# Kernel optimization log

Measured on AMD Instinct MI355X. Metric: run time of the kernel, lower is better.

Reference implementation:

```python
import jax, jax.numpy as jnp
import numpy as np

D_IN = 1024
D_OUT = 1024
NUM_HEADS = 16
HEAD_DIM = D_OUT // NUM_HEADS


def setup_inputs() -> dict:
    key = jax.random.key(0)
    ks = jax.random.split(key, 6)
    s = 0.02
    return {
        "x": jax.random.normal(ks[0], (4, 2048, D_IN), dtype=jnp.float32),
        "Wq": jax.random.normal(ks[1], (D_IN, D_OUT), dtype=jnp.float32) * s,
        "Wk": jax.random.normal(ks[2], (D_IN, D_OUT), dtype=jnp.float32) * s,
        "Wv": jax.random.normal(ks[3], (D_IN, D_OUT), dtype=jnp.float32) * s,
        "Wo": jax.random.normal(ks[4], (D_OUT, D_OUT), dtype=jnp.float32) * s,
        "bo": jax.random.normal(ks[5], (D_OUT,), dtype=jnp.float32) * s,
    }


def reference(x, Wq, Wk, Wv, Wo, bo):
    B, S, _ = x.shape
    # QKV projections (no bias), split into heads: [B, H, S, Dh]
    def split_heads(t):
        return t.reshape(B, S, NUM_HEADS, HEAD_DIM).transpose(0, 2, 1, 3)

    q = split_heads(x @ Wq)
    k = split_heads(x @ Wk)
    v = split_heads(x @ Wv)

    # causal scores [B, H, S, S]; note: original masks BEFORE scaling,
    # but -inf is scale-invariant so softmax(scores/sqrt(d)) with mask is identical.
    scores = jnp.einsum("bhqd,bhkd->bhqk", q, k) / jnp.sqrt(jnp.asarray(HEAD_DIM, x.dtype))
    causal = jnp.tril(jnp.ones((S, S), dtype=bool))
    scores = jnp.where(causal, scores, -jnp.inf)
    attn = jax.nn.softmax(scores, axis=-1)
    # dropout p=0.0 -> identity
    ctx = jnp.einsum("bhqk,bhkd->bhqd", attn, v)  # [B, H, S, Dh]
    ctx = ctx.transpose(0, 2, 1, 3).reshape(B, S, D_OUT)
    return ctx @ Wo + bo
```

## Files before the change

kernel.cpp:

```cpp
#include <hip/hip_runtime.h>
#include <hip/hip_bf16.h>
#include <math.h>


typedef __attribute__((ext_vector_type(8))) short short8;
typedef __attribute__((ext_vector_type(4))) float f32x4;

#define MFMA_BF16(a, b, c) __builtin_amdgcn_mfma_f32_16x16x32_bf16((a), (b), (c), 0, 0, 0)

__device__ __forceinline__ void gld_lds16(const void* g, void* l) {
  __builtin_amdgcn_global_load_lds((const __attribute__((address_space(1))) void*)g,
                                   (__attribute__((address_space(3))) void*)l, 16, 0, 0);
}

__global__ void cast_f32_bf16(const float* __restrict__ in, __hip_bfloat16* __restrict__ out) {
  int i = blockIdx.x * blockDim.x + threadIdx.x;
  float4 v = ((const float4*)in)[i];
  __align__(8) __hip_bfloat16 tmp[4] = {__float2bfloat16(v.x), __float2bfloat16(v.y),
                                        __float2bfloat16(v.z), __float2bfloat16(v.w)};
  ((ushort4*)out)[i] = *(const ushort4*)tmp;
}

__global__ void transpose_cast_w4(const float* __restrict__ W0, const float* __restrict__ W1,
                                  const float* __restrict__ W2, const float* __restrict__ W3,
                                  __hip_bfloat16* __restrict__ T0, __hip_bfloat16* __restrict__ T1,
                                  __hip_bfloat16* __restrict__ T2, __hip_bfloat16* __restrict__ T3) {
  const int z = blockIdx.z;
  const float* W = (z == 0) ? W0 : (z == 1) ? W1 : (z == 2) ? W2 : W3;
  __hip_bfloat16* Wt = (z == 0) ? T0 : (z == 1) ? T1 : (z == 2) ? T2 : T3;
  __shared__ float tile[32][33];
  int tx = threadIdx.x, ty = threadIdx.y;
  int n0 = blockIdx.x * 32, k0 = blockIdx.y * 32;
#pragma unroll
  for (int i = 0; i < 4; ++i)
    tile[ty + i * 8][tx] = W[(size_t)(k0 + ty + i * 8) * 1024 + n0 + tx];
  __syncthreads();
#pragma unroll
  for (int i = 0; i < 4; ++i)
    Wt[(size_t)(n0 + ty + i * 8) * 1024 + k0 + tx] = __float2bfloat16(tile[tx][ty + i * 8]);
}

__global__ __launch_bounds__(256, 2) void gemm_qkv(
    const __hip_bfloat16* __restrict__ A, const __hip_bfloat16* __restrict__ Bt,
    __hip_bfloat16* __restrict__ q, __hip_bfloat16* __restrict__ k,
    __hip_bfloat16* __restrict__ vT) {
  __shared__ __align__(16) __hip_bfloat16 As[128 * 32];
  __shared__ __align__(16) __hip_bfloat16 Bs[128 * 32];
  const int tid = threadIdx.x;
  const int lane = tid & 63, wid = tid >> 6;
  const int quad = lane >> 4, l16 = lane & 15;
  const int part = blockIdx.x >> 3;
  const int n0 = (blockIdx.x & 7) * 128;
  const int gn0 = part * 1024 + n0;
  const int m0 = blockIdx.y * 128;
  const int wm = (wid & 1) * 64, wn = (wid >> 1) * 64;

  f32x4 acc[4][4] = {};

  for (int k0 = 0; k0 < 1024; k0 += 32) {
    __syncthreads();
#pragma unroll
    for (int i = 0; i < 2; ++i) {
      int sbase = __builtin_amdgcn_readfirstlane(wid * 64 + i * 256);
      int s = sbase + lane;
      int row = s >> 2, ch = s & 3;
      gld_lds16(A + (size_t)(m0 + row) * 1024 + k0 + ch * 8, &As[sbase * 8]);
      gld_lds16(Bt + (size_t)(gn0 + row) * 1024 + k0 + ch * 8, &Bs[sbase * 8]);
    }
    __syncthreads();

    short8 af[4], bfr[4];
#pragma unroll
    for (int t = 0; t < 4; ++t) {
      af[t] = *(const short8*)&As[(wm + t * 16 + l16) * 32 + quad * 8];
      bfr[t] = *(const short8*)&Bs[(wn + t * 16 + l16) * 32 + quad * 8];
    }
#pragma unroll
    for (int mt = 0; mt < 4; ++mt)
#pragma unroll
      for (int nt = 0; nt < 4; ++nt)
        acc[mt][nt] = MFMA_BF16(af[mt], bfr[nt], acc[mt][nt]);
  }

  const float CSCL = 0.18033688011112042f;
  if (part < 2) {
    __hip_bfloat16* C = (part == 0) ? q : k;
    const float scl = (part == 0) ? CSCL : 1.0f;
#pragma unroll
    for (int mt = 0; mt < 4; ++mt)
#pragma unroll
      for (int nt = 0; nt < 4; ++nt) {
        int row = m0 + wm + mt * 16 + quad * 4;
        int col = n0 + wn + nt * 16 + l16;
#pragma unroll
        for (int r = 0; r < 4; ++r)
          C[(size_t)(row + r) * 1024 + col] = __float2bfloat16(acc[mt][nt][r] * scl);
      }
  } else {
#pragma unroll
    for (int mt = 0; mt < 4; ++mt)
#pragma unroll
      for (int nt = 0; nt < 4; ++nt) {
        int row = m0 + wm + mt * 16 + quad * 4;
        int nn = n0 + wn + nt * 16 + l16;
        __align__(8) __hip_bfloat16 p4[4];
#pragma unroll
        for (int r = 0; r < 4; ++r) p4[r] = __float2bfloat16(acc[mt][nt][r]);
        *(ushort4*)(vT + (size_t)nn * 8192 + row) = *(const ushort4*)p4;
      }
  }
}

__global__ __launch_bounds__(256, 2) void gemm_bt_f32out(
    const __hip_bfloat16* __restrict__ A, const __hip_bfloat16* __restrict__ Bt,
    float* __restrict__ C, const float* __restrict__ bias, int M, int N, int K) {
  __shared__ __align__(16) __hip_bfloat16 As[128 * 32];
  __shared__ __align__(16) __hip_bfloat16 Bs[128 * 32];
  const int tid = threadIdx.x;
  const int lane = tid & 63, wid = tid >> 6;
  const int quad = lane >> 4, l16 = lane & 15;
  const int m0 = blockIdx.y * 128, n0 = blockIdx.x * 128;
  const int wm = (wid & 1) * 64, wn = (wid >> 1) * 64;

  f32x4 acc[4][4] = {};

  for (int k0 = 0; k0 < K; k0 += 32) {
    __syncthreads();
#pragma unroll
    for (int i = 0; i < 2; ++i) {
      int sbase = __builtin_amdgcn_readfirstlane(wid * 64 + i * 256);
      int s = sbase + lane;
      int row = s >> 2, ch = s & 3;
      gld_lds16(A + (size_t)(m0 + row) * K + k0 + ch * 8, &As[sbase * 8]);
      gld_lds16(Bt + (size_t)(n0 + row) * K + k0 + ch * 8, &Bs[sbase * 8]);
    }
    __syncthreads();

    short8 af[4], bfr[4];
#pragma unroll
    for (int t = 0; t < 4; ++t) {
      af[t] = *(const short8*)&As[(wm + t * 16 + l16) * 32 + quad * 8];
      bfr[t] = *(const short8*)&Bs[(wn + t * 16 + l16) * 32 + quad * 8];
    }
#pragma unroll
    for (int mt = 0; mt < 4; ++mt)
#pragma unroll
      for (int nt = 0; nt < 4; ++nt)
        acc[mt][nt] = MFMA_BF16(af[mt], bfr[nt], acc[mt][nt]);
  }

#pragma unroll
  for (int mt = 0; mt < 4; ++mt)
#pragma unroll
    for (int nt = 0; nt < 4; ++nt) {
      int row = m0 + wm + mt * 16 + quad * 4;
      int col = n0 + wn + nt * 16 + l16;
      float b = bias[col];
#pragma unroll
      for (int r = 0; r < 4; ++r)
        C[(size_t)(row + r) * N + col] = acc[mt][nt][r] + b;
    }
}

__global__ __launch_bounds__(256, 2) void attn_kernel(
    const __hip_bfloat16* __restrict__ Q, const __hip_bfloat16* __restrict__ Km,
    const __hip_bfloat16* __restrict__ vT, __hip_bfloat16* __restrict__ ctx) {
  const int bid = blockIdx.x;
  const int p = bid & 7, h = (bid >> 3) & 15, b = bid >> 7;
  const size_t rbase = (size_t)b * 2048;
  const int tid = threadIdx.x, lane = tid & 63, wid = tid >> 6;
  const int quad = lane >> 4, l16 = lane & 15;

  __shared__ __align__(16) __hip_bfloat16 Ks[64 * 72];
  __shared__ __align__(16) __hip_bfloat16 Vs[64 * 72];
  __shared__ __align__(16) __hip_bfloat16 Ps[4][32 * 76];

  const float NEG_BIG = -1e30f;

#pragma unroll 1
  for (int sub = 0; sub < 2; ++sub) {
    const int qt = sub ? (15 - p) : p;
    const int q0 = qt * 128;

    short8 qf[2][2];
#pragma unroll
    for (int mt = 0; mt < 2; ++mt)
#pragma unroll
      for (int kc = 0; kc < 2; ++kc)
        qf[mt][kc] = *(const short8*)(Q + (rbase + q0 + wid * 32 + mt * 16 + l16) * 1024 +
                                      h * 64 + kc * 32 + quad * 8);

    f32x4 o[2][4] = {};
    f32x4 lp[2] = {};
    const int wave_max_row = q0 + wid * 32 + 31;
    const int ktiles = q0 / 64 + 2;

#pragma unroll 1
    for (int kt = 0; kt < ktiles; ++kt) {
      const int kbase = kt * 64;
      __syncthreads();
      {
#pragma unroll
        for (int i = 0; i < 2; ++i) {
          int s = tid + i * 256;
          int krow = s >> 3, ch = s & 7;
          *(short8*)&Ks[krow * 72 + ch * 8] =
              *(const short8*)(Km + (rbase + kbase + krow) * 1024 + h * 64 + ch * 8);
        }
      }
      {
#pragma unroll
        for (int i = 0; i < 2; ++i) {
          int s = tid + i * 256;
          int d = s >> 3, ch = s & 7;
          *(short8*)&Vs[d * 72 + ch * 8] =
              *(const short8*)(vT + (size_t)(h * 64 + d) * 8192 + rbase + kbase + ch * 8);
        }
      }
      __syncthreads();

      if (kbase <= wave_max_row) {
        short8 kf[4][2];
#pragma unroll
        for (int nt = 0; nt < 4; ++nt)
#pragma unroll
          for (int kc = 0; kc < 2; ++kc)
            kf[nt][kc] = *(const short8*)&Ks[(nt * 16 + l16) * 72 + kc * 32 + quad * 8];
        f32x4 s[2][4];
#pragma unroll
        for (int mt = 0; mt < 2; ++mt)
#pragma unroll
          for (int nt = 0; nt < 4; ++nt) {
            f32x4 sv = {0.f, 0.f, 0.f, 0.f};
            sv = MFMA_BF16(qf[mt][0], kf[nt][0], sv);
            sv = MFMA_BF16(qf[mt][1], kf[nt][1], sv);
            s[mt][nt] = sv;
          }
        if (kbase + 63 > q0 + wid * 32) {
#pragma unroll
          for (int mt = 0; mt < 2; ++mt)
#pragma unroll
            for (int nt = 0; nt < 4; ++nt)
#pragma unroll
              for (int r = 0; r < 4; ++r) {
                int row = q0 + wid * 32 + mt * 16 + quad * 4 + r;
                int col = kbase + nt * 16 + l16;
                if (col > row) s[mt][nt][r] = NEG_BIG;
              }
        }
#pragma unroll
        for (int mt = 0; mt < 2; ++mt) {
#pragma unroll
          for (int nt = 0; nt < 4; ++nt)
#pragma unroll
            for (int r = 0; r < 4; ++r) {
              float pv = __builtin_amdgcn_exp2f(s[mt][nt][r]);
              s[mt][nt][r] = pv;
              lp[mt][r] += pv;
            }
#pragma unroll
          for (int nt = 0; nt < 4; ++nt)
#pragma unroll
            for (int r = 0; r < 4; ++r)
              Ps[wid][(mt * 16 + quad * 4 + r) * 76 + nt * 16 + l16] =
                  __float2bfloat16(s[mt][nt][r]);
        }
        short8 pa[2][2], vf[4][2];
#pragma unroll
        for (int mt = 0; mt < 2; ++mt)
#pragma unroll
          for (int ch = 0; ch < 2; ++ch)
            pa[mt][ch] = *(const short8*)&Ps[wid][(mt * 16 + l16) * 76 + ch * 32 + quad * 8];
#pragma unroll
        for (int dt = 0; dt < 4; ++dt)
#pragma unroll
          for (int ch = 0; ch < 2; ++ch)
            vf[dt][ch] = *(const short8*)&Vs[(dt * 16 + l16) * 72 + ch * 32 + quad * 8];
#pragma unroll
        for (int mt = 0; mt < 2; ++mt)
#pragma unroll
          for (int dt = 0; dt < 4; ++dt) {
            o[mt][dt] = MFMA_BF16(pa[mt][0], vf[dt][0], o[mt][dt]);
            o[mt][dt] = MFMA_BF16(pa[mt][1], vf[dt][1], o[mt][dt]);
          }
      }
    }

#pragma unroll
    for (int mt = 0; mt < 2; ++mt) {
#pragma unroll
      for (int msk = 1; msk <= 8; msk <<= 1)
#pragma unroll
        for (int r = 0; r < 4; ++r)
          lp[mt][r] += __shfl_xor(lp[mt][r], msk, 64);
      float inv[4];
#pragma unroll
      for (int r = 0; r < 4; ++r) inv[r] = 1.f / lp[mt][r];
#pragma unroll
      for (int dt = 0; dt < 4; ++dt)
#pragma unroll
        for (int r = 0; r < 4; ++r)
          ctx[(rbase + q0 + wid * 32 + mt * 16 + quad * 4 + r) * 1024 + h * 64 + dt * 16 + l16] =
              __float2bfloat16(o[mt][dt][r] * inv[r]);
    }
  }
}

extern "C" void kernel_launch(void* const* d_in, const int* in_sizes, int n_in,
                              void* d_out, int out_size, void* d_ws, size_t ws_size,
                              hipStream_t stream) {
  const float* x  = (const float*)d_in[0];
  const float* Wq = (const float*)d_in[1];
  const float* Wk = (const float*)d_in[2];
  const float* Wv = (const float*)d_in[3];
  const float* Wo = (const float*)d_in[4];
  const float* bo = (const float*)d_in[5];
  float* out = (float*)d_out;

  char* ws = (char*)d_ws;
  const size_t MB = 1024ull * 1024ull;
  __hip_bfloat16* q   = (__hip_bfloat16*)(ws);
  __hip_bfloat16* k   = (__hip_bfloat16*)(ws + 16 * MB);
  __hip_bfloat16* vT  = (__hip_bfloat16*)(ws + 32 * MB);
  __hip_bfloat16* woT = (__hip_bfloat16*)(ws + 48 * MB);
  __hip_bfloat16* ctx = q;

  char* outc = (char*)d_out;
  __hip_bfloat16* xb    = (__hip_bfloat16*)(outc);
  __hip_bfloat16* wcatT = (__hip_bfloat16*)(outc + 16 * MB);

  cast_f32_bf16<<<8192, 256, 0, stream>>>(x, xb);
  transpose_cast_w4<<<dim3(32, 32, 4), dim3(32, 8), 0, stream>>>(
      Wq, Wk, Wv, Wo, wcatT, wcatT + 1024 * 1024, wcatT + 2048 * 1024, woT);

  gemm_qkv<<<dim3(24, 64), 256, 0, stream>>>(xb, wcatT, q, k, vT);

  attn_kernel<<<512, 256, 0, stream>>>(q, k, vT, ctx);

  gemm_bt_f32out<<<dim3(8, 64), 256, 0, stream>>>(ctx, woT, out, bo, 8192, 1024, 1024);
}
```

Before: 260.9 us.

## Double GEMM K-tile to 64 with XOR-swizzled LDS and fuse prep kernels

Both bf16 GEMMs now stage 64-wide K slices per iteration instead of 32, halving the number of barrier pairs per tile. An XOR swizzle on the 16-byte chunk index is applied both when loading into LDS and when reading fragments, to avoid bank conflicts caused by the wider row stride. Separately, the x cast and the weight transpose-cast are merged into one launch to save a kernel launch. LDS use per block doubles, which may affect occupancy under the two-blocks-per-CU bound.

```diff
diff --git a/kernel.cpp b/kernel.cpp
--- a/kernel.cpp
+++ b/kernel.cpp
@@ -13,39 +13,42 @@
                                    (__attribute__((address_space(3))) void*)l, 16, 0, 0);
 }
 
-__global__ void cast_f32_bf16(const float* __restrict__ in, __hip_bfloat16* __restrict__ out) {
-  int i = blockIdx.x * blockDim.x + threadIdx.x;
-  float4 v = ((const float4*)in)[i];
-  __align__(8) __hip_bfloat16 tmp[4] = {__float2bfloat16(v.x), __float2bfloat16(v.y),
-                                        __float2bfloat16(v.z), __float2bfloat16(v.w)};
-  ((ushort4*)out)[i] = *(const ushort4*)tmp;
-}
-
-__global__ void transpose_cast_w4(const float* __restrict__ W0, const float* __restrict__ W1,
-                                  const float* __restrict__ W2, const float* __restrict__ W3,
-                                  __hip_bfloat16* __restrict__ T0, __hip_bfloat16* __restrict__ T1,
-                                  __hip_bfloat16* __restrict__ T2, __hip_bfloat16* __restrict__ T3) {
-  const int z = blockIdx.z;
-  const float* W = (z == 0) ? W0 : (z == 1) ? W1 : (z == 2) ? W2 : W3;
-  __hip_bfloat16* Wt = (z == 0) ? T0 : (z == 1) ? T1 : (z == 2) ? T2 : T3;
-  __shared__ float tile[32][33];
-  int tx = threadIdx.x, ty = threadIdx.y;
-  int n0 = blockIdx.x * 32, k0 = blockIdx.y * 32;
-#pragma unroll
-  for (int i = 0; i < 4; ++i)
-    tile[ty + i * 8][tx] = W[(size_t)(k0 + ty + i * 8) * 1024 + n0 + tx];
-  __syncthreads();
-#pragma unroll
-  for (int i = 0; i < 4; ++i)
-    Wt[(size_t)(n0 + ty + i * 8) * 1024 + k0 + tx] = __float2bfloat16(tile[tx][ty + i * 8]);
+__global__ void prep_kernel(const float* __restrict__ x, __hip_bfloat16* __restrict__ xb,
+                            const float* __restrict__ W0, const float* __restrict__ W1,
+                            const float* __restrict__ W2, const float* __restrict__ W3,
+                            __hip_bfloat16* __restrict__ T0, __hip_bfloat16* __restrict__ T1,
+                            __hip_bfloat16* __restrict__ T2, __hip_bfloat16* __restrict__ T3) {
+  const int bid = blockIdx.x, tid = threadIdx.x;
+  if (bid < 8192) {
+    int i = bid * 256 + tid;
+    float4 v = ((const float4*)x)[i];
+    __align__(8) __hip_bfloat16 tmp[4] = {__float2bfloat16(v.x), __float2bfloat16(v.y),
+                                          __float2bfloat16(v.z), __float2bfloat16(v.w)};
+    ((ushort4*)xb)[i] = *(const ushort4*)tmp;
+  } else {
+    int zz = bid - 8192;
+    int z = zz >> 10, rem = zz & 1023;
+    const float* W = (z == 0) ? W0 : (z == 1) ? W1 : (z == 2) ? W2 : W3;
+    __hip_bfloat16* Wt = (z == 0) ? T0 : (z == 1) ? T1 : (z == 2) ? T2 : T3;
+    __shared__ float tile[32][33];
+    int tx = tid & 31, ty = tid >> 5;
+    int n0 = (rem & 31) * 32, k0 = (rem >> 5) * 32;
+#pragma unroll
+    for (int i = 0; i < 4; ++i)
+      tile[ty + i * 8][tx] = W[(size_t)(k0 + ty + i * 8) * 1024 + n0 + tx];
+    __syncthreads();
+#pragma unroll
+    for (int i = 0; i < 4; ++i)
+      Wt[(size_t)(n0 + ty + i * 8) * 1024 + k0 + tx] = __float2bfloat16(tile[tx][ty + i * 8]);
+  }
 }
 
 __global__ __launch_bounds__(256, 2) void gemm_qkv(
     const __hip_bfloat16* __restrict__ A, const __hip_bfloat16* __restrict__ Bt,
     __hip_bfloat16* __restrict__ q, __hip_bfloat16* __restrict__ k,
     __hip_bfloat16* __restrict__ vT) {
-  __shared__ __align__(16) __hip_bfloat16 As[128 * 32];
-  __shared__ __align__(16) __hip_bfloat16 Bs[128 * 32];
+  __shared__ __align__(16) __hip_bfloat16 As[128 * 64];
+  __shared__ __align__(16) __hip_bfloat16 Bs[128 * 64];
   const int tid = threadIdx.x;
   const int lane = tid & 63, wid = tid >> 6;
   const int quad = lane >> 4, l16 = lane & 15;
@@ -54,32 +57,39 @@
   const int gn0 = part * 1024 + n0;
   const int m0 = blockIdx.y * 128;
   const int wm = (wid & 1) * 64, wn = (wid >> 1) * 64;
+  const int swz = l16 & 7;
 
   f32x4 acc[4][4] = {};
 
-  for (int k0 = 0; k0 < 1024; k0 += 32) {
-    __syncthreads();
-#pragma unroll
-    for (int i = 0; i < 2; ++i) {
-      int sbase = __builtin_amdgcn_readfirstlane(wid * 64 + i * 256);
+  for (int k0 = 0; k0 < 1024; k0 += 64) {
+    __syncthreads();
+#pragma unroll
+    for (int i = 0; i < 4; ++i) {
+      int sbase = __builtin_amdgcn_readfirstlane(wid * 256 + i * 64);
       int s = sbase + lane;
-      int row = s >> 2, ch = s & 3;
+      int row = s >> 3;
+      int ch = (s & 7) ^ (row & 7);
       gld_lds16(A + (size_t)(m0 + row) * 1024 + k0 + ch * 8, &As[sbase * 8]);
       gld_lds16(Bt + (size_t)(gn0 + row) * 1024 + k0 + ch * 8, &Bs[sbase * 8]);
     }
     __syncthreads();
 
-    short8 af[4], bfr[4];
-#pragma unroll
-    for (int t = 0; t < 4; ++t) {
-      af[t] = *(const short8*)&As[(wm + t * 16 + l16) * 32 + quad * 8];
-      bfr[t] = *(const short8*)&Bs[(wn + t * 16 + l16) * 32 + quad * 8];
-    }
-#pragma unroll
-    for (int mt = 0; mt < 4; ++mt)
-#pragma unroll
-      for (int nt = 0; nt < 4; ++nt)
-        acc[mt][nt] = MFMA_BF16(af[mt], bfr[nt], acc[mt][nt]);
+    short8 af[4][2], bfr[4][2];
+#pragma unroll
+    for (int t = 0; t < 4; ++t)
+#pragma unroll
+      for (int kc = 0; kc < 2; ++kc) {
+        int chp = (kc * 4 + quad) ^ swz;
+        af[t][kc]  = *(const short8*)&As[(wm + t * 16 + l16) * 64 + chp * 8];
+        bfr[t][kc] = *(const short8*)&Bs[(wn + t * 16 + l16) * 64 + chp * 8];
+      }
+#pragma unroll
+    for (int kc = 0; kc < 2; ++kc)
+#pragma unroll
+      for (int mt = 0; mt < 4; ++mt)
+#pragma unroll
+        for (int nt = 0; nt < 4; ++nt)
+          acc[mt][nt] = MFMA_BF16(af[mt][kc], bfr[nt][kc], acc[mt][nt]);
   }
 
   const float CSCL = 0.18033688011112042f;
@@ -114,39 +124,46 @@
 __global__ __launch_bounds__(256, 2) void gemm_bt_f32out(
     const __hip_bfloat16* __restrict__ A, const __hip_bfloat16* __restrict__ Bt,
     float* __restrict__ C, const float* __restrict__ bias, int M, int N, int K) {
-  __shared__ __align__(16) __hip_bfloat16 As[128 * 32];
-  __shared__ __align__(16) __hip_bfloat16 Bs[128 * 32];
+  __shared__ __align__(16) __hip_bfloat16 As[128 * 64];
+  __shared__ __align__(16) __hip_bfloat16 Bs[128 * 64];
   const int tid = threadIdx.x;
   const int lane = tid & 63, wid = tid >> 6;
   const int quad = lane >> 4, l16 = lane & 15;
   const int m0 = blockIdx.y * 128, n0 = blockIdx.x * 128;
   const int wm = (wid & 1) * 64, wn = (wid >> 1) * 64;
+  const int swz = l16 & 7;
 
   f32x4 acc[4][4] = {};
 
-  for (int k0 = 0; k0 < K; k0 += 32) {
-    __syncthreads();
-#pragma unroll
-    for (int i = 0; i < 2; ++i) {
-      int sbase = __builtin_amdgcn_readfirstlane(wid * 64 + i * 256);
+  for (int k0 = 0; k0 < K; k0 += 64) {
+    __syncthreads();
+#pragma unroll
+    for (int i = 0; i < 4; ++i) {
+      int sbase = __builtin_amdgcn_readfirstlane(wid * 256 + i * 64);
       int s = sbase + lane;
-      int row = s >> 2, ch = s & 3;
+      int row = s >> 3;
+      int ch = (s & 7) ^ (row & 7);
       gld_lds16(A + (size_t)(m0 + row) * K + k0 + ch * 8, &As[sbase * 8]);
       gld_lds16(Bt + (size_t)(n0 + row) * K + k0 + ch * 8, &Bs[sbase * 8]);
     }
     __syncthreads();
 
-    short8 af[4], bfr[4];
-#pragma unroll
-    for (int t = 0; t < 4; ++t) {
-      af[t] = *(const short8*)&As[(wm + t * 16 + l16) * 32 + quad * 8];
-      bfr[t] = *(const short8*)&Bs[(wn + t * 16 + l16) * 32 + quad * 8];
-    }
-#pragma unroll
-    for (int mt = 0; mt < 4; ++mt)
-#pragma unroll
-      for (int nt = 0; nt < 4; ++nt)
-        acc[mt][nt] = MFMA_BF16(af[mt], bfr[nt], acc[mt][nt]);
+    short8 af[4][2], bfr[4][2];
+#pragma unroll
+    for (int t = 0; t < 4; ++t)
+#pragma unroll
+      for (int kc = 0; kc < 2; ++kc) {
+        int chp = (kc * 4 + quad) ^ swz;
+        af[t][kc]  = *(const short8*)&As[(wm + t * 16 + l16) * 64 + chp * 8];
+        bfr[t][kc] = *(const short8*)&Bs[(wn + t * 16 + l16) * 64 + chp * 8];
+      }
+#pragma unroll
+    for (int kc = 0; kc < 2; ++kc)
+#pragma unroll
+      for (int mt = 0; mt < 4; ++mt)
+#pragma unroll
+        for (int nt = 0; nt < 4; ++nt)
+          acc[mt][nt] = MFMA_BF16(af[mt][kc], bfr[nt][kc], acc[mt][nt]);
   }
 
 #pragma unroll
@@ -329,9 +346,9 @@
   __hip_bfloat16* xb    = (__hip_bfloat16*)(outc);
   __hip_bfloat16* wcatT = (__hip_bfloat16*)(outc + 16 * MB);
 
-  cast_f32_bf16<<<8192, 256, 0, stream>>>(x, xb);
-  transpose_cast_w4<<<dim3(32, 32, 4), dim3(32, 8), 0, stream>>>(
-      Wq, Wk, Wv, Wo, wcatT, wcatT + 1024 * 1024, wcatT + 2048 * 1024, woT);
+  prep_kernel<<<8192 + 4096, 256, 0, stream>>>(
+      x, xb, Wq, Wk, Wv, Wo,
+      wcatT, wcatT + 1024 * 1024, wcatT + 2048 * 1024, woT);
 
   gemm_qkv<<<dim3(24, 64), 256, 0, stream>>>(xb, wcatT, q, k, vT);
 
```

After: 241.4 us. 7.5% less time.
